# Kernel optimization log

Hardware: AMD Instinct MI355X
Metric: run time of the kernel (lower is better)

## Reference

```python
import jax, jax.numpy as jnp
import numpy as np

H, W = 256, 256
DX, DY = 1.0, 1.0
EI, KC, GC = 1.0, 1.0, 1.0
LAYERS = [2, 256, 512, 1024, H * W]
B = 64


def _d2x(f, dx):
    # reflect-pad width 1 on x (last axis), stencil [1, -2, 1]
    p = jnp.pad(f, ((0, 0), (0, 0), (0, 0), (1, 1)), mode='reflect')
    return (p[..., :-2] - 2.0 * p[..., 1:-1] + p[..., 2:]) / (dx * dx)


def _d2y(f, dy):
    p = jnp.pad(f, ((0, 0), (0, 0), (1, 1), (0, 0)), mode='reflect')
    return (p[:, :, :-2, :] - 2.0 * p[:, :, 1:-1, :] + p[:, :, 2:, :]) / (dy * dy)


def setup_inputs() -> dict:
    key = jax.random.key(0)
    ks = jax.random.split(key, 10)
    inp = {
        'x_coloc': jax.random.normal(ks[0], (B, LAYERS[0]), jnp.float32),
        'P': jax.random.normal(ks[1], (B, H * W), jnp.float32),
    }
    for i in range(4):
        inp[f'W{i + 1}'] = jax.random.normal(ks[2 + i], (LAYERS[i], LAYERS[i + 1]), jnp.float32) / np.sqrt(LAYERS[i]).astype(np.float32)
        inp[f'b{i + 1}'] = jnp.zeros((LAYERS[i + 1],), jnp.float32)
    return inp


def reference(x_coloc, P, W1, b1, W2, b2, W3, b3, W4, b4):
    # MLP field predictor: Linear+ReLU x3, final Linear -> [B, H*W]
    h = jax.nn.relu(x_coloc @ W1 + b1)
    h = jax.nn.relu(h @ W2 + b2)
    h = jax.nn.relu(h @ W3 + b3)
    f = h @ W4 + b4                      # [B, H*W]
    fm = f.reshape(B, 1, H, W)

    fx2 = _d2x(fm, DX)                   # d2/dx2
    fy2 = _d2y(fm, DY)                   # d2/dy2
    lap = fx2 + fy2
    biharmonic = _d2x(lap, DX) + _d2y(lap, DY)

    residual = EI * biharmonic + GC * (fx2 + fy2) + KC * fm - P.reshape(B, 1, H, W)
    return residual.reshape(B, H * W)
```

## Files before the change

### kernel.cpp

```cpp
#include <hip/hip_runtime.h>


#define BATCH 64
#define NPIX 65536

typedef __attribute__((ext_vector_type(8))) short short8_t;
typedef __attribute__((ext_vector_type(4))) float f32x4;

#define LDS_FENCE()   asm volatile("s_waitcnt lgkmcnt(0)" ::: "memory")
#define MEM_ORDER()   asm volatile("" ::: "memory")

__device__ __forceinline__ short f2bf(float x) {
    unsigned u = __float_as_uint(x);
    unsigned r = (u + 0x7fffu + ((u >> 16) & 1u)) >> 16;
    return (short)r;
}

__global__ void k_layer12(const float* __restrict__ x, const float* __restrict__ W1,
                          const float* __restrict__ b1, const float* __restrict__ W2,
                          const float* __restrict__ b2, float* __restrict__ h2) {
    __shared__ float As[16][64];
    __shared__ float Ws[64][16];
    int tid = threadIdx.x;
    int tn = tid & 15, tm = tid >> 4;
    int n0 = blockIdx.x * 16, m0 = blockIdx.y * 16;
    float acc = 0.f;
    for (int k0 = 0; k0 < 256; k0 += 64) {
#pragma unroll
        for (int j = 0; j < 4; ++j) {
            int e = j * 256 + tid;
            int m = m0 + (e >> 6), kk = k0 + (e & 63);
            float v = x[m * 2 + 0] * W1[kk] + x[m * 2 + 1] * W1[256 + kk] + b1[kk];
            As[e >> 6][e & 63] = v > 0.f ? v : 0.f;
        }
#pragma unroll
        for (int j = 0; j < 4; ++j) {
            int e = j * 256 + tid;
            Ws[e >> 4][e & 15] = W2[(k0 + (e >> 4)) * 512 + n0 + (e & 15)];
        }
        __syncthreads();
#pragma unroll
        for (int k = 0; k < 64; ++k)
            acc += As[tm][k] * Ws[k][tn];
        __syncthreads();
    }
    acc += b2[n0 + tn];
    acc = acc > 0.f ? acc : 0.f;
    h2[(m0 + tm) * 512 + n0 + tn] = acc;
}

__global__ void k_layer3(const float* __restrict__ A, const float* __restrict__ Wt,
                         const float* __restrict__ bias, short* __restrict__ out_bf) {
    __shared__ float As[16][64];
    __shared__ float Ws[64][16];
    int tid = threadIdx.x;
    int tn = tid & 15, tm = tid >> 4;
    int n0 = blockIdx.x * 16, m0 = blockIdx.y * 16;
    float acc = 0.f;
    for (int k0 = 0; k0 < 512; k0 += 64) {
#pragma unroll
        for (int j = 0; j < 4; ++j) {
            int e = j * 256 + tid;
            As[e >> 6][e & 63] = A[(m0 + (e >> 6)) * 512 + k0 + (e & 63)];
        }
#pragma unroll
        for (int j = 0; j < 4; ++j) {
            int e = j * 256 + tid;
            Ws[e >> 4][e & 15] = Wt[(k0 + (e >> 4)) * 1024 + n0 + (e & 15)];
        }
        __syncthreads();
#pragma unroll
        for (int k = 0; k < 64; ++k)
            acc += As[tm][k] * Ws[k][tn];
        __syncthreads();
    }
    acc += bias[n0 + tn];
    acc = acc > 0.f ? acc : 0.f;
    out_bf[(m0 + tm) * 1024 + n0 + tn] = f2bf(acc);
}

__global__ __launch_bounds__(64) void k_gemm_mfma(
        const short* __restrict__ A,
        const float* __restrict__ W,
        const float* __restrict__ bias,
        float* __restrict__ f) {
    __shared__ float Bl[32 * 64];
    const int lane = threadIdx.x;
    const int lr = lane & 15;
    const int g = lane >> 4;
    const int n0w = blockIdx.x * 64;

    f32x4 acc[4][4];
#pragma unroll
    for (int a = 0; a < 4; ++a)
#pragma unroll
        for (int b = 0; b < 4; ++b)
            acc[a][b] = {0.f, 0.f, 0.f, 0.f};

    const short* ap = A + lr * 1024 + g * 8;

    f32x4 RA[8], RB[8];
    const int kof = lane >> 4;
    const int cof = (lane & 15) * 4;

    auto gloadA = [&](int k0) {
#pragma unroll
        for (int i = 0; i < 8; ++i)
            RA[i] = *(const f32x4*)(W + (size_t)(k0 + i * 4 + kof) * NPIX + n0w + cof);
    };
    auto gloadB = [&](int k0) {
#pragma unroll
        for (int i = 0; i < 8; ++i)
            RB[i] = *(const f32x4*)(W + (size_t)(k0 + i * 4 + kof) * NPIX + n0w + cof);
    };
    auto lwriteA = [&]() {
#pragma unroll
        for (int i = 0; i < 8; ++i) {
            int k = i * 4 + kof;
            int cc = cof ^ (((i >> 1) & 3) << 4);
            *(f32x4*)&Bl[k * 64 + cc] = RA[i];
        }
    };
    auto lwriteB = [&]() {
#pragma unroll
        for (int i = 0; i < 8; ++i) {
            int k = i * 4 + kof;
            int cc = cof ^ (((i >> 1) & 3) << 4);
            *(f32x4*)&Bl[k * 64 + cc] = RB[i];
        }
    };

    short8_t aC[4], aN[4];

    auto compute = [&](int ) {
#pragma unroll
        for (int t = 0; t < 4; ++t) {
            const int csw = (t * 16 + lr) ^ (g << 4);
            short8_t bf;
#pragma unroll
            for (int j = 0; j < 8; ++j)
                bf[j] = f2bf(Bl[(g * 8 + j) * 64 + csw]);
#pragma unroll
            for (int mt = 0; mt < 4; ++mt)
                acc[mt][t] = __builtin_amdgcn_mfma_f32_16x16x32_bf16(aC[mt], bf, acc[mt][t], 0, 0, 0);
        }
    };
    auto advanceA = [&](int s) {
#pragma unroll
        for (int mt = 0; mt < 4; ++mt) aC[mt] = aN[mt];
        if (s + 2 < 32) {
#pragma unroll
            for (int mt = 0; mt < 4; ++mt)
                aN[mt] = *(const short8_t*)(ap + mt * 16384 + (s + 2) * 32);
        }
    };

    gloadA(0);
    gloadB(32);
#pragma unroll
    for (int mt = 0; mt < 4; ++mt)
        aC[mt] = *(const short8_t*)(ap + mt * 16384);
#pragma unroll
    for (int mt = 0; mt < 4; ++mt)
        aN[mt] = *(const short8_t*)(ap + mt * 16384 + 32);
    lwriteA();
    gloadA(64);
    LDS_FENCE();

    for (int t2 = 0; t2 < 16; ++t2) {
        const int s0 = 2 * t2;
        compute(s0);
        MEM_ORDER();
        if (s0 < 31) {
            lwriteB();
            LDS_FENCE();
            if (s0 < 29) gloadB((s0 + 3) * 32);
        }
        advanceA(s0);
        const int s1 = s0 + 1;
        compute(s1);
        MEM_ORDER();
        if (s1 < 31) {
            lwriteA();
            LDS_FENCE();
            if (s1 < 29) gloadA((s1 + 3) * 32);
        }
        advanceA(s1);
    }

#pragma unroll
    for (int h = 0; h < 2; ++h) {
        MEM_ORDER();
#pragma unroll
        for (int mtl = 0; mtl < 2; ++mtl) {
            int mt = h * 2 + mtl;
#pragma unroll
            for (int t = 0; t < 4; ++t) {
                float bb = bias[n0w + t * 16 + lr];
#pragma unroll
                for (int r = 0; r < 4; ++r)
                    Bl[(mtl * 16 + g * 4 + r) * 64 + t * 16 + lr] = acc[mt][t][r] + bb;
            }
        }
        LDS_FENCE();
#pragma unroll
        for (int jj = 0; jj < 8; ++jj) {
            int rl = jj * 4 + kof;
            f32x4 v = *(const f32x4*)&Bl[rl * 64 + cof];
            *(f32x4*)(f + (size_t)(h * 32 + rl) * NPIX + n0w + cof) = v;
        }
        MEM_ORDER();
    }
}

#define ROWS 16
__device__ __forceinline__ int rfl(int i) {
    return i < 0 ? -i : (i > 255 ? 510 - i : i);
}
__global__ void k_stencil(const float* __restrict__ f, const float* __restrict__ P,
                          float* __restrict__ out) {
    __shared__ float fs[ROWS + 4][256];
    int x = threadIdx.x;
    int y0 = blockIdx.x * ROWS;
    int b = blockIdx.y;
    const float* fb = f + (size_t)b * NPIX;
    for (int t = 0; t < ROWS + 4; ++t) {
        int gy = rfl(y0 - 2 + t);
        fs[t][x] = fb[gy * 256 + x];
    }
    __syncthreads();

    int xm = x == 0 ? 1 : x - 1;
    int xp = x == 255 ? 254 : x + 1;

    auto lapAt = [&](int j, int i) {
        int s = j - y0 + 2;
        int sm = rfl(j - 1) - y0 + 2;
        int sp = rfl(j + 1) - y0 + 2;
        int im = i == 0 ? 1 : i - 1;
        int ip = i == 255 ? 254 : i + 1;
        float c = fs[s][i];
        return (fs[sm][i] - 2.f * c + fs[sp][i]) + (fs[s][im] - 2.f * c + fs[s][ip]);
    };

    for (int r = 0; r < ROWS; ++r) {
        int y = y0 + r;
        float lc = lapAt(y, x);
        float lym = lapAt(rfl(y - 1), x);
        float lyp = lapAt(rfl(y + 1), x);
        float lxm = lapAt(y, xm);
        float lxp = lapAt(y, xp);
        float bih = (lym - 2.f * lc + lyp) + (lxm - 2.f * lc + lxp);
        float fc = fs[r + 2][x];
        size_t idx = (size_t)b * NPIX + y * 256 + x;
        out[idx] = bih + lc + fc - P[idx];
    }
}

extern "C" void kernel_launch(void* const* d_in, const int* in_sizes, int n_in,
                              void* d_out, int out_size, void* d_ws, size_t ws_size,
                              hipStream_t stream) {
    const float* x  = (const float*)d_in[0];
    const float* P  = (const float*)d_in[1];
    const float* W1 = (const float*)d_in[2];
    const float* b1 = (const float*)d_in[3];
    const float* W2 = (const float*)d_in[4];
    const float* b2 = (const float*)d_in[5];
    const float* W3 = (const float*)d_in[6];
    const float* b3 = (const float*)d_in[7];
    const float* W4 = (const float*)d_in[8];
    const float* b4 = (const float*)d_in[9];
    float* out = (float*)d_out;

    char* ws = (char*)d_ws;
    float* h2  = (float*)(ws);
    short* h3b = (short*)(ws + (128 << 10));
    float* f   = (float*)(ws + (256 << 10));

    k_layer12<<<dim3(512 / 16, 4), 256, 0, stream>>>(x, W1, b1, W2, b2, h2);
    k_layer3<<<dim3(1024 / 16, 4), 256, 0, stream>>>(h2, W3, b3, h3b);
    k_gemm_mfma<<<NPIX / 64, 64, 0, stream>>>(h3b, W4, b4, f);
    k_stencil<<<dim3(256 / ROWS, BATCH), 256, 0, stream>>>(f, P, out);
}
```

Baseline: 93.14 us.

## Split K across two waves in W4 GEMM with LDS reduction

The final-layer MFMA GEMM now runs two waves per block. Each wave handles alternating 32-wide K slices using its own LDS staging buffer, and the partial accumulators are reduced through LDS before the bias and store epilogue. The aim is to double the wave count, giving more memory-level parallelism while streaming the large W4 matrix. The cost is an extra LDS reduction plus barriers, and the second wave sits idle during the epilogue.

```diff
diff --git a/kernel.cpp b/kernel.cpp
--- a/kernel.cpp
+++ b/kernel.cpp
@@ -79,16 +79,21 @@
     out_bf[(m0 + tm) * 1024 + n0 + tn] = f2bf(acc);
 }
 
-__global__ __launch_bounds__(64) void k_gemm_mfma(
+__global__ __launch_bounds__(128) void k_gemm_mfma(
         const short* __restrict__ A,
         const float* __restrict__ W,
         const float* __restrict__ bias,
         float* __restrict__ f) {
-    __shared__ float Bl[32 * 64];
-    const int lane = threadIdx.x;
+    __shared__ float Bl[2][32 * 64];
+    const int tid = threadIdx.x;
+    const int wv = tid >> 6;
+    const int lane = tid & 63;
     const int lr = lane & 15;
     const int g = lane >> 4;
     const int n0w = blockIdx.x * 64;
+    const int kof = lane >> 4;
+    const int cof = (lane & 15) * 4;
+    float* Blw = &Bl[wv][0];
 
     f32x4 acc[4][4];
 #pragma unroll
@@ -100,94 +105,121 @@
     const short* ap = A + lr * 1024 + g * 8;
 
     f32x4 RA[8], RB[8];
-    const int kof = lane >> 4;
-    const int cof = (lane & 15) * 4;
-
-    auto gloadA = [&](int k0) {
-#pragma unroll
-        for (int i = 0; i < 8; ++i)
-            RA[i] = *(const f32x4*)(W + (size_t)(k0 + i * 4 + kof) * NPIX + n0w + cof);
-    };
-    auto gloadB = [&](int k0) {
-#pragma unroll
-        for (int i = 0; i < 8; ++i)
-            RB[i] = *(const f32x4*)(W + (size_t)(k0 + i * 4 + kof) * NPIX + n0w + cof);
+    auto gloadA = [&](int i) {
+        const float* wp = W + (size_t)((2 * i + wv) * 32) * NPIX + n0w + cof;
+#pragma unroll
+        for (int q = 0; q < 8; ++q)
+            RA[q] = *(const f32x4*)(wp + (size_t)(q * 4 + kof) * NPIX);
+    };
+    auto gloadB = [&](int i) {
+        const float* wp = W + (size_t)((2 * i + wv) * 32) * NPIX + n0w + cof;
+#pragma unroll
+        for (int q = 0; q < 8; ++q)
+            RB[q] = *(const f32x4*)(wp + (size_t)(q * 4 + kof) * NPIX);
     };
     auto lwriteA = [&]() {
 #pragma unroll
-        for (int i = 0; i < 8; ++i) {
-            int k = i * 4 + kof;
-            int cc = cof ^ (((i >> 1) & 3) << 4);
-            *(f32x4*)&Bl[k * 64 + cc] = RA[i];
+        for (int q = 0; q < 8; ++q) {
+            int k = q * 4 + kof;
+            int cc = cof ^ (((q >> 1) & 3) << 4);
+            *(f32x4*)&Blw[k * 64 + cc] = RA[q];
         }
     };
     auto lwriteB = [&]() {
 #pragma unroll
-        for (int i = 0; i < 8; ++i) {
-            int k = i * 4 + kof;
-            int cc = cof ^ (((i >> 1) & 3) << 4);
-            *(f32x4*)&Bl[k * 64 + cc] = RB[i];
+        for (int q = 0; q < 8; ++q) {
+            int k = q * 4 + kof;
+            int cc = cof ^ (((q >> 1) & 3) << 4);
+            *(f32x4*)&Blw[k * 64 + cc] = RB[q];
         }
     };
 
     short8_t aC[4], aN[4];
 
-    auto compute = [&](int ) {
+    auto compute = [&]() {
 #pragma unroll
         for (int t = 0; t < 4; ++t) {
             const int csw = (t * 16 + lr) ^ (g << 4);
             short8_t bf;
 #pragma unroll
             for (int j = 0; j < 8; ++j)
-                bf[j] = f2bf(Bl[(g * 8 + j) * 64 + csw]);
+                bf[j] = f2bf(Blw[(g * 8 + j) * 64 + csw]);
 #pragma unroll
             for (int mt = 0; mt < 4; ++mt)
                 acc[mt][t] = __builtin_amdgcn_mfma_f32_16x16x32_bf16(aC[mt], bf, acc[mt][t], 0, 0, 0);
         }
     };
-    auto advanceA = [&](int s) {
-#pragma unroll
-        for (int mt = 0; mt < 4; ++mt) aC[mt] = aN[mt];
-        if (s + 2 < 32) {
+    auto advanceA = [&](int i) {
+        if (i + 1 < 16) {
+#pragma unroll
+            for (int mt = 0; mt < 4; ++mt) aC[mt] = aN[mt];
+        }
+        if (i + 2 < 16) {
 #pragma unroll
             for (int mt = 0; mt < 4; ++mt)
-                aN[mt] = *(const short8_t*)(ap + mt * 16384 + (s + 2) * 32);
+                aN[mt] = *(const short8_t*)(ap + mt * 16384 + (2 * (i + 2) + wv) * 32);
         }
     };
 
     gloadA(0);
-    gloadB(32);
+    gloadB(1);
 #pragma unroll
     for (int mt = 0; mt < 4; ++mt)
-        aC[mt] = *(const short8_t*)(ap + mt * 16384);
+        aC[mt] = *(const short8_t*)(ap + mt * 16384 + wv * 32);
 #pragma unroll
     for (int mt = 0; mt < 4; ++mt)
-        aN[mt] = *(const short8_t*)(ap + mt * 16384 + 32);
+        aN[mt] = *(const short8_t*)(ap + mt * 16384 + (2 + wv) * 32);
     lwriteA();
-    gloadA(64);
+    gloadA(2);
     LDS_FENCE();
 
-    for (int t2 = 0; t2 < 16; ++t2) {
-        const int s0 = 2 * t2;
-        compute(s0);
+    for (int t2 = 0; t2 < 8; ++t2) {
+        const int i0 = 2 * t2;
+        compute();
         MEM_ORDER();
-        if (s0 < 31) {
+        if (i0 < 15) {
             lwriteB();
             LDS_FENCE();
-            if (s0 < 29) gloadB((s0 + 3) * 32);
-        }
-        advanceA(s0);
-        const int s1 = s0 + 1;
-        compute(s1);
+            if (i0 < 13) gloadB(i0 + 3);
+        }
+        advanceA(i0);
+        const int i1 = i0 + 1;
+        compute();
         MEM_ORDER();
-        if (s1 < 31) {
+        if (i1 < 15) {
             lwriteA();
             LDS_FENCE();
-            if (s1 < 29) gloadA((s1 + 3) * 32);
-        }
-        advanceA(s1);
-    }
-
+            if (i1 < 13) gloadA(i1 + 3);
+        }
+        advanceA(i1);
+    }
+
+    __syncthreads();
+    if (wv == 1) {
+        float* AccBuf = &Bl[0][0];
+#pragma unroll
+        for (int mt = 0; mt < 4; ++mt)
+#pragma unroll
+            for (int t = 0; t < 4; ++t)
+                *(f32x4*)&AccBuf[(mt * 4 + t) * 256 + lane * 4] = acc[mt][t];
+    }
+    __syncthreads();
+    if (wv == 1) return;
+
+    {
+        float* AccBuf = &Bl[0][0];
+#pragma unroll
+        for (int mt = 0; mt < 4; ++mt)
+#pragma unroll
+            for (int t = 0; t < 4; ++t) {
+                f32x4 o = *(const f32x4*)&AccBuf[(mt * 4 + t) * 256 + lane * 4];
+                acc[mt][t][0] += o[0]; acc[mt][t][1] += o[1];
+                acc[mt][t][2] += o[2]; acc[mt][t][3] += o[3];
+            }
+    }
+    MEM_ORDER();
+
+    float* Ble = &Bl[0][0];
 #pragma unroll
     for (int h = 0; h < 2; ++h) {
         MEM_ORDER();
@@ -199,14 +231,14 @@
                 float bb = bias[n0w + t * 16 + lr];
 #pragma unroll
                 for (int r = 0; r < 4; ++r)
-                    Bl[(mtl * 16 + g * 4 + r) * 64 + t * 16 + lr] = acc[mt][t][r] + bb;
+                    Ble[(mtl * 16 + g * 4 + r) * 64 + t * 16 + lr] = acc[mt][t][r] + bb;
             }
         }
         LDS_FENCE();
 #pragma unroll
         for (int jj = 0; jj < 8; ++jj) {
             int rl = jj * 4 + kof;
-            f32x4 v = *(const f32x4*)&Bl[rl * 64 + cof];
+            f32x4 v = *(const f32x4*)&Ble[rl * 64 + cof];
             *(f32x4*)(f + (size_t)(h * 32 + rl) * NPIX + n0w + cof) = v;
         }
         MEM_ORDER();
@@ -279,6 +311,6 @@
 
     k_layer12<<<dim3(512 / 16, 4), 256, 0, stream>>>(x, W1, b1, W2, b2, h2);
     k_layer3<<<dim3(1024 / 16, 4), 256, 0, stream>>>(h2, W3, b3, h3b);
-    k_gemm_mfma<<<NPIX / 64, 64, 0, stream>>>(h3b, W4, b4, f);
+    k_gemm_mfma<<<NPIX / 64, 128, 0, stream>>>(h3b, W4, b4, f);
     k_stencil<<<dim3(256 / ROWS, BATCH), 256, 0, stream>>>(f, P, out);
 }
```

Result: no change. 94.02 us (+0.9%).
